# Performance work log

Hardware: AMD Instinct MI355X
Metric: run time of the kernel (lower is better)

## Reference

```python
import jax, jax.numpy as jnp
import numpy as np
import math

D_IN = 1024
D_OUT = 1024
NUM_HEADS = 16
HEAD_DIM = D_OUT // NUM_HEADS
B = 2
S = 4096


def setup_inputs() -> dict:
    key = jax.random.key(0)
    ks = jax.random.split(key, 6)
    x = jax.random.normal(ks[0], (B, S, D_IN), dtype=jnp.float32)
    # kaiming-uniform-ish scale for weights; exact init values don't matter for correctness
    bound = 1.0 / math.sqrt(D_IN)
    Wq = jax.random.uniform(ks[1], (D_OUT, D_IN), minval=-bound, maxval=bound, dtype=jnp.float32)
    Wk = jax.random.uniform(ks[2], (D_OUT, D_IN), minval=-bound, maxval=bound, dtype=jnp.float32)
    Wv = jax.random.uniform(ks[3], (D_OUT, D_IN), minval=-bound, maxval=bound, dtype=jnp.float32)
    Wo = jax.random.uniform(ks[4], (D_OUT, D_OUT), minval=-bound, maxval=bound, dtype=jnp.float32)
    bo = jax.random.uniform(ks[5], (D_OUT,), minval=-bound, maxval=bound, dtype=jnp.float32)
    return {"x": x, "Wq": Wq, "Wk": Wk, "Wv": Wv, "Wo": Wo, "bo": bo}


@jax.custom_vjp
def binarize(w):
    return jnp.sign(w)

def _bin_fwd(w):
    return jnp.sign(w), w

def _bin_bwd(w, g):
    # straight-through estimator: pass grad where |w| <= 1
    return (g * (jnp.abs(w) <= 1).astype(g.dtype),)

binarize.defvjp(_bin_fwd, _bin_bwd)


def reference(x, Wq, Wk, Wv, Wo, bo):
    b, n, _ = x.shape
    h, hd = NUM_HEADS, HEAD_DIM
    # binarized projections (torch F.linear: x @ W.T)
    q = (x @ binarize(Wq).T).reshape(b, n, h, hd).transpose(0, 2, 1, 3)  # [b,h,n,hd]
    k = (x @ binarize(Wk).T).reshape(b, n, h, hd).transpose(0, 2, 1, 3)
    v = (x @ binarize(Wv).T).reshape(b, n, h, hd).transpose(0, 2, 1, 3)
    scores = jnp.einsum('bhqd,bhkd->bhqk', q, k) / math.sqrt(hd)  # [b,h,n,n]
    causal = jnp.tril(jnp.ones((n, n), dtype=bool))
    scores = jnp.where(causal, scores, -jnp.inf)
    attn = jax.nn.softmax(scores, axis=-1)
    # dropout p=0.0 -> identity
    ctx = jnp.einsum('bhqk,bhkd->bqhd', attn, v).reshape(b, n, h * hd)
    return ctx @ binarize(Wo).T + bo
```

## Files before the change

### kernel.cpp

```cpp
#include <hip/hip_runtime.h>
#include <hip/hip_bf16.h>
#include <cstdint>
#include <cstddef>

#define S 4096
#define D 1024
#define H 16
#define HD 64
#define BATCH 2
#define M_TOK 8192
#define K2 2048

typedef short short8 __attribute__((ext_vector_type(8)));
typedef __bf16 bf16x8 __attribute__((ext_vector_type(8)));
typedef float f32x4 __attribute__((ext_vector_type(4)));
typedef unsigned int u32;

static __device__ __forceinline__ ushort f2bf(float f) {
  union { float f; uint32_t u; } v; v.f = f;
  uint32_t u = v.u + 0x7FFFu + ((v.u >> 16) & 1u);
  return (ushort)(u >> 16);
}
static __device__ __forceinline__ float bf2f(ushort h) {
  union { uint32_t u; float f; } v; v.u = ((uint32_t)h) << 16; return v.f;
}
static __device__ __forceinline__ uint32_t cvtpk(float lo, float hi) {
  uint32_t r;
  asm("v_cvt_pk_bf16_f32 %0, %1, %2" : "=v"(r) : "v"(lo), "v"(hi));
  return r;
}
static __device__ __forceinline__ float vexp2(float x) {
  float r;
  asm("v_exp_f32 %0, %1" : "=v"(r) : "v"(x));
  return r;
}
static __device__ __forceinline__ bf16x8 pack4(uint32_t a, uint32_t b, uint32_t c, uint32_t d) {
  union { uint32_t u[4]; bf16x8 v; } z;
  z.u[0] = a; z.u[1] = b; z.u[2] = c; z.u[3] = d;
  return z.v;
}
static __device__ __forceinline__ void gld16(const void* g, void* l) {
  __builtin_amdgcn_global_load_lds(
      (const __attribute__((address_space(1))) u32*)g,
      (__attribute__((address_space(3))) u32*)l, 16, 0, 0);
}
static __device__ __forceinline__ ushort sgn(float a) {
  return a > 0.f ? 0x3F80 : (a < 0.f ? 0xBF80 : 0);
}

__global__ void prep_x(const float* __restrict__ x, ushort* __restrict__ xcat) {
  int i = blockIdx.x * blockDim.x + threadIdx.x;
  const int total = M_TOK * 128;
  for (; i < total; i += gridDim.x * blockDim.x) {
    int row = i >> 7, c8 = (i & 127) * 8;
    const float* px = &x[(size_t)row * 1024 + c8];
    float4 a = *(const float4*)px;
    float4 b = *(const float4*)(px + 4);
    float va[8] = {a.x, a.y, a.z, a.w, b.x, b.y, b.z, b.w};
    union { ushort u[8]; short8 v; } Hh, Ll;
#pragma unroll
    for (int j = 0; j < 8; ++j) {
      ushort h = f2bf(va[j]);
      Hh.u[j] = h;
      Ll.u[j] = f2bf(va[j] - bf2f(h));
    }
    *(short8*)&xcat[(size_t)row * K2 + c8] = Hh.v;
    *(short8*)&xcat[(size_t)row * K2 + 1024 + c8] = Ll.v;
  }
}

__global__ void prep_w(const float* __restrict__ wq, const float* __restrict__ wk,
                       const float* __restrict__ wv, const float* __restrict__ wo,
                       ushort* __restrict__ wcat, ushort* __restrict__ wob) {
  int i = blockIdx.x * blockDim.x + threadIdx.x;
  const int total = (D * D) / 4;
  for (; i < total; i += gridDim.x * blockDim.x) {
    float4 a;
    union { ushort u[4]; uint2 v; } t;
    a = *(const float4*)&wq[i * 4];
    t.u[0] = sgn(a.x); t.u[1] = sgn(a.y); t.u[2] = sgn(a.z); t.u[3] = sgn(a.w);
    *(uint2*)&wcat[i * 4] = t.v;
    a = *(const float4*)&wk[i * 4];
    t.u[0] = sgn(a.x); t.u[1] = sgn(a.y); t.u[2] = sgn(a.z); t.u[3] = sgn(a.w);
    *(uint2*)&wcat[D * D + i * 4] = t.v;
    a = *(const float4*)&wv[i * 4];
    t.u[0] = sgn(a.x); t.u[1] = sgn(a.y); t.u[2] = sgn(a.z); t.u[3] = sgn(a.w);
    *(uint2*)&wcat[2 * D * D + i * 4] = t.v;
    a = *(const float4*)&wo[i * 4];
    t.u[0] = sgn(a.x); t.u[1] = sgn(a.y); t.u[2] = sgn(a.z); t.u[3] = sgn(a.w);
    *(uint2*)&wob[i * 4] = t.v;
  }
}

template<int EPI, int KK, int BROW>
__global__ __launch_bounds__(256) void gemm97(
    const ushort* __restrict__ A, const ushort* __restrict__ Bw,
    ushort* __restrict__ q_hi, ushort* __restrict__ q_lo,
    ushort* __restrict__ k_hi, ushort* __restrict__ k_lo,
    ushort* __restrict__ v_t,
    float* __restrict__ of, const float* __restrict__ bias)
{
  __shared__ ushort smA[128 * 32];
  __shared__ ushort smB[128 * 32];
  const int tid = threadIdx.x;
  const int l = tid & 63;
  const int w = tid >> 6;
  const int x = l & 15, g = l >> 4;
  const int wm = w >> 1, wn = w & 1;
  const int bm = blockIdx.x, bn = blockIdx.y;

  const ushort* gA[2]; const ushort* gB[2]; int ldso[2];
#pragma unroll
  for (int p = 0; p < 2; ++p) {
    int q = p * 256 + tid;
    gA[p] = &A[(size_t)(bm * 128 + (q >> 2)) * KK + (q & 3) * 8];
    gB[p] = &Bw[(size_t)(bn * 128 + (q >> 2)) * BROW + (q & 3) * 8];
    ldso[p] = (p * 256 + w * 64) * 8;
  }

  f32x4 acc[4][4] = {};

  for (int k0 = 0; k0 < KK; k0 += 32) {
    __syncthreads();
#pragma unroll
    for (int p = 0; p < 2; ++p) {
      gld16(gA[p] + k0, &smA[ldso[p]]);
      gld16(gB[p] + (k0 & (BROW - 1)), &smB[ldso[p]]);
    }
    __syncthreads();
    bf16x8 af[4], bf_[4];
#pragma unroll
    for (int m = 0; m < 4; ++m)
      af[m] = *(const bf16x8*)&smA[(wm * 64 + m * 16 + x) * 32 + g * 8];
#pragma unroll
    for (int n = 0; n < 4; ++n)
      bf_[n] = *(const bf16x8*)&smB[(wn * 64 + n * 16 + x) * 32 + g * 8];
#pragma unroll
    for (int m = 0; m < 4; ++m)
#pragma unroll
      for (int n = 0; n < 4; ++n)
        acc[m][n] = __builtin_amdgcn_mfma_f32_16x16x32_bf16(af[m], bf_[n], acc[m][n], 0, 0, 0);
  }

  if (EPI == 0) {
    const int proj = bn >> 3;
    ushort* oh = (proj == 0) ? q_hi : k_hi;
    ushort* ol = (proj == 0) ? q_lo : k_lo;
#pragma unroll
    for (int m = 0; m < 4; ++m)
#pragma unroll
      for (int n = 0; n < 4; ++n)
#pragma unroll
        for (int r = 0; r < 4; ++r) {
          int rowg = bm * 128 + wm * 64 + m * 16 + g * 4 + r;
          int colg = bn * 128 + wn * 64 + n * 16 + x;
          float v = acc[m][n][r];
          int bi = rowg >> 12, ntok = rowg & 4095;
          int cg = colg & 1023;
          int h = cg >> 6, hd = cg & 63;
          size_t bhb = (size_t)(bi * H + h) * (S * HD);
          if (proj < 2) {
            size_t off = bhb + (size_t)ntok * HD + hd;
            ushort hiv = f2bf(v);
            oh[off] = hiv;
            ol[off] = f2bf(v - bf2f(hiv));
          } else {
            int t5 = ntok & 31;
            int pos = ((t5 >> 2) & 3) * 8 + ((t5 >> 4) & 1) * 4 + (t5 & 3);
            v_t[bhb + (size_t)hd * S + (ntok & ~31) + pos] = f2bf(v);
          }
        }
  } else {
#pragma unroll
    for (int m = 0; m < 4; ++m)
#pragma unroll
      for (int n = 0; n < 4; ++n)
#pragma unroll
        for (int r = 0; r < 4; ++r) {
          int rowg = bm * 128 + wm * 64 + m * 16 + g * 4 + r;
          int colg = bn * 128 + wn * 64 + n * 16 + x;
          of[(size_t)rowg * D + colg] = acc[m][n][r] + bias[colg];
        }
  }
}

__global__ __launch_bounds__(256) void flash9(
    const ushort* __restrict__ qhi, const ushort* __restrict__ qlo,
    const ushort* __restrict__ khi, const ushort* __restrict__ klo,
    const ushort* __restrict__ vt, ushort* __restrict__ ctx)
{
  __shared__ ushort smKhi[3][64 * 64];
  __shared__ ushort smKlo[3][64 * 64];
  __shared__ ushort smVT[3][64 * 64];

  const int tid = threadIdx.x;
  const int l = tid & 63;
  const int w = tid >> 6;
  const int x = l & 15;
  const int g = l >> 4;
  const int bh = blockIdx.x;
  const int qt = (int)(gridDim.y - 1) - (int)blockIdx.y;
  const int qbase = qt * 128;
  const size_t qkbase = (size_t)bh * S * HD;

  const int rr = tid >> 2;
  int soff_k[2]; size_t soff_v[2]; int ldso[2];
#pragma unroll
  for (int p = 0; p < 2; ++p) {
    int q = p * 256 + tid;
    int r2 = q >> 3;
    int sb = (q & 7) ^ (r2 & 7);
    soff_k[p] = r2 * HD + sb * 8;
    soff_v[p] = (size_t)r2 * S + sb * 8;
    ldso[p] = (p * 256 + w * 64) * 8;
  }
  const ushort* khb = khi + qkbase;
  const ushort* klb = klo + qkbase;
  const ushort* vtb = vt + qkbase;

  bf16x8 bq[2][2][2];
#pragma unroll
  for (int qs = 0; qs < 2; ++qs) {
    int qrow = qbase + w * 32 + qs * 16 + x;
    size_t base = qkbase + (size_t)qrow * HD + g * 8;
    bq[qs][0][0] = *(const bf16x8*)&qhi[base];
    bq[qs][0][1] = *(const bf16x8*)&qhi[base + 32];
    bq[qs][1][0] = *(const bf16x8*)&qlo[base];
    bq[qs][1][1] = *(const bf16x8*)&qlo[base + 32];
  }

  float mrun[2] = {-1e30f, -1e30f};
  float lrun[2] = {0.f, 0.f};
  f32x4 oacc[2][4] = {};

  const int kvmax = (qbase + 127) >> 6;
  const int qmaxw = qbase + w * 32 + 31;
  const float C1 = 0.125f * 1.44269504f;
  const float TH = 8.0f / C1;

#pragma unroll
  for (int p = 0; p < 2; ++p) {
    gld16(khb + soff_k[p], &smKhi[0][ldso[p]]);
    gld16(klb + soff_k[p], &smKlo[0][ldso[p]]);
    gld16(vtb + soff_v[p], &smVT[0][ldso[p]]);
  }

  int cb = 0;
  for (int kv = 0; kv <= kvmax; ++kv) {
    if (kv < kvmax) {
      const ushort* kh = khb + (size_t)(kv + 1) * (64 * HD);
      const ushort* kl = klb + (size_t)(kv + 1) * (64 * HD);
      const ushort* vp = vtb + (size_t)(kv + 1) * 64;
      int nb = (cb == 2) ? 0 : cb + 1;
#pragma unroll
      for (int p = 0; p < 2; ++p) {
        gld16(kh + soff_k[p], &smKhi[nb][ldso[p]]);
        gld16(kl + soff_k[p], &smKlo[nb][ldso[p]]);
        gld16(vp + soff_v[p], &smVT[nb][ldso[p]]);
      }
      asm volatile("s_waitcnt vmcnt(6)" ::: "memory");
    } else {
      asm volatile("s_waitcnt vmcnt(0)" ::: "memory");
    }
    __builtin_amdgcn_s_barrier();

    if (kv * 64 <= qmaxw) {
      const ushort* bKhi = smKhi[cb];
      const ushort* bKlo = smKlo[cb];
      const ushort* bVT = smVT[cb];

      f32x4 scq[2][4];
      __builtin_amdgcn_s_setprio(1);
#pragma unroll
      for (int t = 0; t < 4; ++t) {
        f32x4 a0 = {}, a1 = {};
#pragma unroll
        for (int c = 0; c < 2; ++c) {
          int pb = (t * 16 + x) * 64 + ((4 * c + g) ^ (x & 7)) * 8;
          bf16x8 kH = *(const bf16x8*)&bKhi[pb];
          bf16x8 kL = *(const bf16x8*)&bKlo[pb];
          a0 = __builtin_amdgcn_mfma_f32_16x16x32_bf16(kH, bq[0][0][c], a0, 0, 0, 0);
          a0 = __builtin_amdgcn_mfma_f32_16x16x32_bf16(kL, bq[0][0][c], a0, 0, 0, 0);
          a0 = __builtin_amdgcn_mfma_f32_16x16x32_bf16(kH, bq[0][1][c], a0, 0, 0, 0);
          a1 = __builtin_amdgcn_mfma_f32_16x16x32_bf16(kH, bq[1][0][c], a1, 0, 0, 0);
          a1 = __builtin_amdgcn_mfma_f32_16x16x32_bf16(kL, bq[1][0][c], a1, 0, 0, 0);
          a1 = __builtin_amdgcn_mfma_f32_16x16x32_bf16(kH, bq[1][1][c], a1, 0, 0, 0);
        }
        scq[0][t] = a0; scq[1][t] = a1;
      }
      __builtin_amdgcn_s_setprio(0);

      const bool needmask = (kv * 64 + 63 > qbase + w * 32);
      uint32_t pbq[2][2][4];

#pragma unroll
      for (int qs = 0; qs < 2; ++qs) {
        if (needmask) {
          int qglob = qbase + w * 32 + qs * 16 + x;
          int kb = kv * 64 + 4 * g;
#pragma unroll
          for (int t = 0; t < 4; ++t)
#pragma unroll
            for (int r = 0; r < 4; ++r)
              if (kb + t * 16 + r > qglob) scq[qs][t][r] = -1e30f;
        }
        float mt[4];
#pragma unroll
        for (int t = 0; t < 4; ++t)
          mt[t] = fmaxf(fmaxf(scq[qs][t][0], scq[qs][t][1]),
                        fmaxf(scq[qs][t][2], scq[qs][t][3]));
        float mloc = fmaxf(fmaxf(mt[0], mt[1]), fmaxf(mt[2], mt[3]));
        if (__any(mloc > mrun[qs] + TH)) {
          mloc = fmaxf(mloc, __shfl_xor(mloc, 16));
          mloc = fmaxf(mloc, __shfl_xor(mloc, 32));
          float mnew = fmaxf(mrun[qs], mloc);
          float scal = vexp2((mrun[qs] - mnew) * C1);
          mrun[qs] = mnew;
          lrun[qs] *= scal;
#pragma unroll
          for (int dt = 0; dt < 4; ++dt) oacc[qs][dt] *= scal;
        }
        float mc = mrun[qs] * C1;
#pragma unroll
        for (int t = 0; t < 4; ++t)
#pragma unroll
          for (int r = 0; r < 4; ++r)
            scq[qs][t][r] = vexp2(scq[qs][t][r] * C1 - mc);
        float st[4];
#pragma unroll
        for (int t = 0; t < 4; ++t)
          st[t] = (scq[qs][t][0] + scq[qs][t][1]) + (scq[qs][t][2] + scq[qs][t][3]);
        lrun[qs] += (st[0] + st[1]) + (st[2] + st[3]);
#pragma unroll
        for (int c = 0; c < 2; ++c) {
          pbq[qs][c][0] = cvtpk(scq[qs][2 * c][0], scq[qs][2 * c][1]);
          pbq[qs][c][1] = cvtpk(scq[qs][2 * c][2], scq[qs][2 * c][3]);
          pbq[qs][c][2] = cvtpk(scq[qs][2 * c + 1][0], scq[qs][2 * c + 1][1]);
          pbq[qs][c][3] = cvtpk(scq[qs][2 * c + 1][2], scq[qs][2 * c + 1][3]);
        }
      }

      __builtin_amdgcn_s_setprio(1);
#pragma unroll
      for (int c = 0; c < 2; ++c)
#pragma unroll
        for (int dt = 0; dt < 4; ++dt) {
          bf16x8 vf = *(const bf16x8*)&bVT[(dt * 16 + x) * 64 + ((4 * c + g) ^ (x & 7)) * 8];
          oacc[0][dt] = __builtin_amdgcn_mfma_f32_16x16x32_bf16(
              vf, pack4(pbq[0][c][0], pbq[0][c][1], pbq[0][c][2], pbq[0][c][3]), oacc[0][dt], 0, 0, 0);
          oacc[1][dt] = __builtin_amdgcn_mfma_f32_16x16x32_bf16(
              vf, pack4(pbq[1][c][0], pbq[1][c][1], pbq[1][c][2], pbq[1][c][3]), oacc[1][dt], 0, 0, 0);
        }
      __builtin_amdgcn_s_setprio(0);
    }

    cb = (cb == 2) ? 0 : cb + 1;
  }

  const int b = bh >> 4, h = bh & 15;
#pragma unroll
  for (int qs = 0; qs < 2; ++qs) {
    float ls = lrun[qs];
    ls += __shfl_xor(ls, 16);
    ls += __shfl_xor(ls, 32);
    float inv = 1.0f / ls;
    int tok = qbase + w * 32 + qs * 16 + x;
#pragma unroll
    for (int dt = 0; dt < 4; ++dt) {
      uint2 uu;
      uu.x = cvtpk(oacc[qs][dt][0] * inv, oacc[qs][dt][1] * inv);
      uu.y = cvtpk(oacc[qs][dt][2] * inv, oacc[qs][dt][3] * inv);
      *(uint2*)&ctx[(size_t)(b * S + tok) * D + h * 64 + dt * 16 + 4 * g] = uu;
    }
  }
}

extern "C" void kernel_launch(void* const* d_in, const int* in_sizes, int n_in,
                              void* d_out, int out_size, void* d_ws, size_t ws_size,
                              hipStream_t stream) {
  const float* x  = (const float*)d_in[0];
  const float* Wq = (const float*)d_in[1];
  const float* Wk = (const float*)d_in[2];
  const float* Wv = (const float*)d_in[3];
  const float* Wo = (const float*)d_in[4];
  const float* bo = (const float*)d_in[5];
  float* out = (float*)d_out;

  if (ws_size < (size_t)120 * 1024 * 1024) return;

  char* ws = (char*)d_ws;
  const size_t MB = 1024 * 1024;
  ushort* xcat = (ushort*)(ws);
  ushort* ctx  = (ushort*)(ws);
  ushort* wcat = (ushort*)(ws + 32 * MB);
  ushort* wob  = (ushort*)(ws + 38 * MB);
  ushort* qhi  = (ushort*)(ws + 40 * MB);
  ushort* qlo  = (ushort*)(ws + 56 * MB);
  ushort* khi  = (ushort*)(ws + 72 * MB);
  ushort* klo  = (ushort*)(ws + 88 * MB);
  ushort* vt   = (ushort*)(ws + 104 * MB);

  prep_x<<<2048, 256, 0, stream>>>(x, xcat);
  prep_w<<<1024, 256, 0, stream>>>(Wq, Wk, Wv, Wo, wcat, wob);

  gemm97<0, K2, 1024><<<dim3(64, 24), 256, 0, stream>>>(
      xcat, wcat, qhi, qlo, khi, klo, vt, nullptr, nullptr);

  flash9<<<dim3(BATCH * H, S / 128), 256, 0, stream>>>(qhi, qlo, khi, klo, vt, ctx);

  gemm97<2, 1024, 1024><<<dim3(64, 8), 256, 0, stream>>>(
      ctx, wob, nullptr, nullptr, nullptr, nullptr, nullptr, out, bo);
}
```

Baseline: 341.8 us.

## Software-pipeline flash attention PV with next QK; split V projection to single-K GEMM

The attention loop is restructured so the P·V MFMAs for the previous KV tile run between the QK score MFMAs and the softmax of the current tile. This lets the matrix work overlap the exp/max VALU work, and a trailing PV step is added after the loop. Separately, the V projection moves into its own GEMM launch that uses only the hi half of K (K=1024) instead of the full 2048 split-precision K. That cuts redundant MFMA work for V at the cost of an extra launch. The pipelining keeps P fragments live across iterations, which raises register pressure.

```diff
diff --git a/kernel.cpp b/kernel.cpp
--- a/kernel.cpp
+++ b/kernel.cpp
@@ -92,7 +92,7 @@
   }
 }
 
-template<int EPI, int KK, int BROW>
+template<int EPI, int KK, int BROW, int AST>
 __global__ __launch_bounds__(256) void gemm97(
     const ushort* __restrict__ A, const ushort* __restrict__ Bw,
     ushort* __restrict__ q_hi, ushort* __restrict__ q_lo,
@@ -113,7 +113,7 @@
 #pragma unroll
   for (int p = 0; p < 2; ++p) {
     int q = p * 256 + tid;
-    gA[p] = &A[(size_t)(bm * 128 + (q >> 2)) * KK + (q & 3) * 8];
+    gA[p] = &A[(size_t)(bm * 128 + (q >> 2)) * AST + (q & 3) * 8];
     gB[p] = &Bw[(size_t)(bn * 128 + (q >> 2)) * BROW + (q & 3) * 8];
     ldso[p] = (p * 256 + w * 64) * 8;
   }
@@ -142,24 +142,26 @@
         acc[m][n] = __builtin_amdgcn_mfma_f32_16x16x32_bf16(af[m], bf_[n], acc[m][n], 0, 0, 0);
   }
 
-  if (EPI == 0) {
-    const int proj = bn >> 3;
-    ushort* oh = (proj == 0) ? q_hi : k_hi;
-    ushort* ol = (proj == 0) ? q_lo : k_lo;
-#pragma unroll
-    for (int m = 0; m < 4; ++m)
-#pragma unroll
-      for (int n = 0; n < 4; ++n)
-#pragma unroll
-        for (int r = 0; r < 4; ++r) {
-          int rowg = bm * 128 + wm * 64 + m * 16 + g * 4 + r;
-          int colg = bn * 128 + wn * 64 + n * 16 + x;
-          float v = acc[m][n][r];
+#pragma unroll
+  for (int m = 0; m < 4; ++m)
+#pragma unroll
+    for (int n = 0; n < 4; ++n)
+#pragma unroll
+      for (int r = 0; r < 4; ++r) {
+        int rowg = bm * 128 + wm * 64 + m * 16 + g * 4 + r;
+        int colg = bn * 128 + wn * 64 + n * 16 + x;
+        float v = acc[m][n][r];
+        if (EPI == 2) {
+          of[(size_t)rowg * D + colg] = v + bias[colg];
+        } else {
           int bi = rowg >> 12, ntok = rowg & 4095;
           int cg = colg & 1023;
           int h = cg >> 6, hd = cg & 63;
           size_t bhb = (size_t)(bi * H + h) * (S * HD);
-          if (proj < 2) {
+          if (EPI == 0) {
+            const int proj = bn >> 3;
+            ushort* oh = (proj == 0) ? q_hi : k_hi;
+            ushort* ol = (proj == 0) ? q_lo : k_lo;
             size_t off = bhb + (size_t)ntok * HD + hd;
             ushort hiv = f2bf(v);
             oh[off] = hiv;
@@ -170,21 +172,10 @@
             v_t[bhb + (size_t)hd * S + (ntok & ~31) + pos] = f2bf(v);
           }
         }
-  } else {
-#pragma unroll
-    for (int m = 0; m < 4; ++m)
-#pragma unroll
-      for (int n = 0; n < 4; ++n)
-#pragma unroll
-        for (int r = 0; r < 4; ++r) {
-          int rowg = bm * 128 + wm * 64 + m * 16 + g * 4 + r;
-          int colg = bn * 128 + wn * 64 + n * 16 + x;
-          of[(size_t)rowg * D + colg] = acc[m][n][r] + bias[colg];
-        }
-  }
-}
-
-__global__ __launch_bounds__(256) void flash9(
+      }
+}
+
+__global__ __launch_bounds__(256) void flash10(
     const ushort* __restrict__ qhi, const ushort* __restrict__ qlo,
     const ushort* __restrict__ khi, const ushort* __restrict__ klo,
     const ushort* __restrict__ vt, ushort* __restrict__ ctx)
@@ -203,7 +194,6 @@
   const int qbase = qt * 128;
   const size_t qkbase = (size_t)bh * S * HD;
 
-  const int rr = tid >> 2;
   int soff_k[2]; size_t soff_v[2]; int ldso[2];
 #pragma unroll
   for (int p = 0; p < 2; ++p) {
@@ -232,9 +222,10 @@
   float mrun[2] = {-1e30f, -1e30f};
   float lrun[2] = {0.f, 0.f};
   f32x4 oacc[2][4] = {};
+  uint32_t pbq[2][2][4];
 
   const int kvmax = (qbase + 127) >> 6;
-  const int qmaxw = qbase + w * 32 + 31;
+  const int kw = (qbase + w * 32 + 31) >> 6;
   const float C1 = 0.125f * 1.44269504f;
   const float TH = 8.0f / C1;
 
@@ -245,7 +236,7 @@
     gld16(vtb + soff_v[p], &smVT[0][ldso[p]]);
   }
 
-  int cb = 0;
+  int cb = 0, pvb = 2;
   for (int kv = 0; kv <= kvmax; ++kv) {
     if (kv < kvmax) {
       const ushort* kh = khb + (size_t)(kv + 1) * (64 * HD);
@@ -264,12 +255,13 @@
     }
     __builtin_amdgcn_s_barrier();
 
-    if (kv * 64 <= qmaxw) {
+    const bool doQK = (kv <= kw);
+    const bool doPV = (kv >= 1) && (kv - 1 <= kw);
+
+    f32x4 scq[2][4];
+    if (doQK) {
       const ushort* bKhi = smKhi[cb];
       const ushort* bKlo = smKlo[cb];
-      const ushort* bVT = smVT[cb];
-
-      f32x4 scq[2][4];
       __builtin_amdgcn_s_setprio(1);
 #pragma unroll
       for (int t = 0; t < 4; ++t) {
@@ -289,10 +281,11 @@
         scq[0][t] = a0; scq[1][t] = a1;
       }
       __builtin_amdgcn_s_setprio(0);
-
+    }
+
+    float mloc[2];
+    if (doQK) {
       const bool needmask = (kv * 64 + 63 > qbase + w * 32);
-      uint32_t pbq[2][2][4];
-
 #pragma unroll
       for (int qs = 0; qs < 2; ++qs) {
         if (needmask) {
@@ -309,37 +302,12 @@
         for (int t = 0; t < 4; ++t)
           mt[t] = fmaxf(fmaxf(scq[qs][t][0], scq[qs][t][1]),
                         fmaxf(scq[qs][t][2], scq[qs][t][3]));
-        float mloc = fmaxf(fmaxf(mt[0], mt[1]), fmaxf(mt[2], mt[3]));
-        if (__any(mloc > mrun[qs] + TH)) {
-          mloc = fmaxf(mloc, __shfl_xor(mloc, 16));
-          mloc = fmaxf(mloc, __shfl_xor(mloc, 32));
-          float mnew = fmaxf(mrun[qs], mloc);
-          float scal = vexp2((mrun[qs] - mnew) * C1);
-          mrun[qs] = mnew;
-          lrun[qs] *= scal;
-#pragma unroll
-          for (int dt = 0; dt < 4; ++dt) oacc[qs][dt] *= scal;
-        }
-        float mc = mrun[qs] * C1;
-#pragma unroll
-        for (int t = 0; t < 4; ++t)
-#pragma unroll
-          for (int r = 0; r < 4; ++r)
-            scq[qs][t][r] = vexp2(scq[qs][t][r] * C1 - mc);
-        float st[4];
-#pragma unroll
-        for (int t = 0; t < 4; ++t)
-          st[t] = (scq[qs][t][0] + scq[qs][t][1]) + (scq[qs][t][2] + scq[qs][t][3]);
-        lrun[qs] += (st[0] + st[1]) + (st[2] + st[3]);
-#pragma unroll
-        for (int c = 0; c < 2; ++c) {
-          pbq[qs][c][0] = cvtpk(scq[qs][2 * c][0], scq[qs][2 * c][1]);
-          pbq[qs][c][1] = cvtpk(scq[qs][2 * c][2], scq[qs][2 * c][3]);
-          pbq[qs][c][2] = cvtpk(scq[qs][2 * c + 1][0], scq[qs][2 * c + 1][1]);
-          pbq[qs][c][3] = cvtpk(scq[qs][2 * c + 1][2], scq[qs][2 * c + 1][3]);
-        }
-      }
-
+        mloc[qs] = fmaxf(fmaxf(mt[0], mt[1]), fmaxf(mt[2], mt[3]));
+      }
+    }
+
+    if (doPV) {
+      const ushort* bVT = smVT[pvb];
       __builtin_amdgcn_s_setprio(1);
 #pragma unroll
       for (int c = 0; c < 2; ++c)
@@ -354,7 +322,57 @@
       __builtin_amdgcn_s_setprio(0);
     }
 
+    if (doQK) {
+#pragma unroll
+      for (int qs = 0; qs < 2; ++qs) {
+        if (__any(mloc[qs] > mrun[qs] + TH)) {
+          float mx = mloc[qs];
+          mx = fmaxf(mx, __shfl_xor(mx, 16));
+          mx = fmaxf(mx, __shfl_xor(mx, 32));
+          float mnew = fmaxf(mrun[qs], mx);
+          float scal = vexp2((mrun[qs] - mnew) * C1);
+          mrun[qs] = mnew;
+          lrun[qs] *= scal;
+#pragma unroll
+          for (int dt = 0; dt < 4; ++dt) oacc[qs][dt] *= scal;
+        }
+        float mc = mrun[qs] * C1;
+#pragma unroll
+        for (int t = 0; t < 4; ++t)
+#pragma unroll
+          for (int r = 0; r < 4; ++r)
+            scq[qs][t][r] = vexp2(scq[qs][t][r] * C1 - mc);
+        float st[4];
+#pragma unroll
+        for (int t = 0; t < 4; ++t)
+          st[t] = (scq[qs][t][0] + scq[qs][t][1]) + (scq[qs][t][2] + scq[qs][t][3]);
+        lrun[qs] += (st[0] + st[1]) + (st[2] + st[3]);
+#pragma unroll
+        for (int c = 0; c < 2; ++c) {
+          pbq[qs][c][0] = cvtpk(scq[qs][2 * c][0], scq[qs][2 * c][1]);
+          pbq[qs][c][1] = cvtpk(scq[qs][2 * c][2], scq[qs][2 * c][3]);
+          pbq[qs][c][2] = cvtpk(scq[qs][2 * c + 1][0], scq[qs][2 * c + 1][1]);
+          pbq[qs][c][3] = cvtpk(scq[qs][2 * c + 1][2], scq[qs][2 * c + 1][3]);
+        }
+      }
+    }
+
+    pvb = cb;
     cb = (cb == 2) ? 0 : cb + 1;
+  }
+
+  if (kw == kvmax) {
+    const ushort* bVT = smVT[pvb];
+#pragma unroll
+    for (int c = 0; c < 2; ++c)
+#pragma unroll
+      for (int dt = 0; dt < 4; ++dt) {
+        bf16x8 vf = *(const bf16x8*)&bVT[(dt * 16 + x) * 64 + ((4 * c + g) ^ (x & 7)) * 8];
+        oacc[0][dt] = __builtin_amdgcn_mfma_f32_16x16x32_bf16(
+            vf, pack4(pbq[0][c][0], pbq[0][c][1], pbq[0][c][2], pbq[0][c][3]), oacc[0][dt], 0, 0, 0);
+        oacc[1][dt] = __builtin_amdgcn_mfma_f32_16x16x32_bf16(
+            vf, pack4(pbq[1][c][0], pbq[1][c][1], pbq[1][c][2], pbq[1][c][3]), oacc[1][dt], 0, 0, 0);
+      }
   }
 
   const int b = bh >> 4, h = bh & 15;
@@ -403,11 +421,13 @@
   prep_x<<<2048, 256, 0, stream>>>(x, xcat);
   prep_w<<<1024, 256, 0, stream>>>(Wq, Wk, Wv, Wo, wcat, wob);
 
-  gemm97<0, K2, 1024><<<dim3(64, 24), 256, 0, stream>>>(
-      xcat, wcat, qhi, qlo, khi, klo, vt, nullptr, nullptr);
-
-  flash9<<<dim3(BATCH * H, S / 128), 256, 0, stream>>>(qhi, qlo, khi, klo, vt, ctx);
-
-  gemm97<2, 1024, 1024><<<dim3(64, 8), 256, 0, stream>>>(
+  gemm97<0, 2048, 1024, 2048><<<dim3(64, 16), 256, 0, stream>>>(
+      xcat, wcat, qhi, qlo, khi, klo, nullptr, nullptr, nullptr);
+  gemm97<1, 1024, 1024, 2048><<<dim3(64, 8), 256, 0, stream>>>(
+      xcat, wcat + 2 * D * D, nullptr, nullptr, nullptr, nullptr, vt, nullptr, nullptr);
+
+  flash10<<<dim3(BATCH * H, S / 128), 256, 0, stream>>>(qhi, qlo, khi, klo, vt, ctx);
+
+  gemm97<2, 1024, 1024, 1024><<<dim3(64, 8), 256, 0, stream>>>(
       ctx, wob, nullptr, nullptr, nullptr, nullptr, nullptr, out, bo);
 }
```

After: 349.9 us. 2.4% more time.
